# Optimization experiments

Measured on AMD Instinct MI355X. Metric: run time of the kernel, lower is better.

Reference implementation:

```python
import jax, jax.numpy as jnp
import numpy as np

B, S, H, I, C = 1024, 512, 128, 1, 10


def _uniform(key, shape, fan):
    stdv = 1.0 / np.sqrt(fan)
    return jax.random.uniform(key, shape, jnp.float32, -stdv, stdv)


def setup_inputs() -> dict:
    key = jax.random.key(0)
    ks = jax.random.split(key, 16)
    return {
        "x": jax.random.normal(ks[0], (B, S), jnp.float32),
        "W_gx": _uniform(ks[1], (I, H), H),
        "W_gh": _uniform(ks[2], (H, H), H),
        "W_ix": _uniform(ks[3], (I, H), H),
        "W_ih": _uniform(ks[4], (H, H), H),
        "W_fx": _uniform(ks[5], (I, H), H),
        "W_fh": _uniform(ks[6], (H, H), H),
        "W_ox": _uniform(ks[7], (I, H), H),
        "W_oh": _uniform(ks[8], (H, H), H),
        "W_ph": _uniform(ks[9], (H, C), C),
        "b_g": _uniform(ks[10], (H,), 1),
        "b_i": _uniform(ks[11], (H,), 1),
        "b_f": _uniform(ks[12], (H,), 1),
        "b_o": _uniform(ks[13], (H,), 1),
        "b_p": _uniform(ks[14], (C,), 1),
    }


def reference(x, W_gx, W_gh, W_ix, W_ih, W_fx, W_fh, W_ox, W_oh, W_ph,
              b_g, b_i, b_f, b_o, b_p):
    Hd = W_gh.shape[0]
    # Fuse the four per-gate GEMMs into one (same math, concatenated weights).
    Wx = jnp.concatenate([W_gx, W_ix, W_fx, W_ox], axis=1)   # [I, 4H]
    Wh = jnp.concatenate([W_gh, W_ih, W_fh, W_oh], axis=1)   # [H, 4H]
    b = jnp.concatenate([b_g, b_i, b_f, b_o])                # [4H]
    # input_dim == 1: timestep t input is x[:, t:t+1] -> xs: [S, B, 1]
    xs = jnp.swapaxes(x[:, :, None], 0, 1)
    # Precompute all input projections in one big GEMM: [S, B, 4H]
    xp = xs @ Wx + b

    def step(carry, xp_t):
        h, c = carry
        gates = xp_t + h @ Wh                    # [B, 4H]
        g = jnp.tanh(gates[:, :Hd])
        i = jax.nn.sigmoid(gates[:, Hd:2 * Hd])
        f = jax.nn.sigmoid(gates[:, 2 * Hd:3 * Hd])
        o = jax.nn.sigmoid(gates[:, 3 * Hd:])
        c_t = g * i + c * f
        h_t = jnp.tanh(c_t) * o
        return (h_t, c_t), None

    h0 = jnp.zeros((x.shape[0], Hd), x.dtype)
    (h_last, _), _ = jax.lax.scan(step, (h0, h0), xp)
    return h_last @ W_ph + b_p                   # logits at final timestep
```

## Files before the change

kernel.cpp:

```cpp
#include <hip/hip_runtime.h>

#define S_LEN 512
#define H_DIM 128
#define C_DIM 10

typedef __attribute__((ext_vector_type(8))) short short8;
typedef __attribute__((ext_vector_type(4))) float f32x4;

__device__ __forceinline__ unsigned short f2bf(float f) {
    union { float f; unsigned u; } v; v.f = f;
    return (unsigned short)((v.u + 0x7FFFu + ((v.u >> 16) & 1u)) >> 16);
}

__device__ __forceinline__ float fast_sigmoid(float x) {
    float e = __builtin_amdgcn_exp2f(-1.4426950408889634f * x);
    return __builtin_amdgcn_rcpf(1.0f + e);
}
__device__ __forceinline__ float fast_tanh(float x) {
    float e = __builtin_amdgcn_exp2f(2.8853900817779268f * x);
    return 1.0f - 2.0f * __builtin_amdgcn_rcpf(e + 1.0f);
}

__global__ __launch_bounds__(512, 2) void lstm_fused(
    const float* __restrict__ x,
    const float* __restrict__ Wgx, const float* __restrict__ Wgh,
    const float* __restrict__ Wix, const float* __restrict__ Wih,
    const float* __restrict__ Wfx, const float* __restrict__ Wfh,
    const float* __restrict__ Wox, const float* __restrict__ Woh,
    const float* __restrict__ Wph,
    const float* __restrict__ bg, const float* __restrict__ bi,
    const float* __restrict__ bff, const float* __restrict__ bo,
    const float* __restrict__ bp,
    float* __restrict__ out)
{
    __shared__ float xT[S_LEN][5];
    __shared__ __attribute__((aligned(16))) unsigned short hb[2][4][136];
    __shared__ float hfin[4][H_DIM];

    const int tid  = threadIdx.x;
    const int lane = tid & 63;
    const int w    = tid >> 6;
    const int b0   = blockIdx.x * 4;

    {
        const float* xp = x + b0 * S_LEN + tid;
        #pragma unroll
        for (int r = 0; r < 4; ++r) xT[tid][r] = xp[r * S_LEN];
    }
    {
        unsigned short* hz = &hb[0][0][0];
        for (int i2 = tid; i2 < 4 * 136; i2 += 512) hz[i2] = 0;
    }

    const int jl = lane & 15;
    const int kg = lane >> 4;
    const int j  = w * 16 + jl;

    const float* WhA[4] = { Wgh, Wih, Wfh, Woh };
    short8 bfrag[4][4];
    #pragma unroll
    for (int g = 0; g < 4; ++g) {
        #pragma unroll
        for (int kk = 0; kk < 4; ++kk) {
            const float* src = WhA[g] + (kk * 32 + kg * 8) * H_DIM + j;
            short8 v;
            #pragma unroll
            for (int e = 0; e < 8; ++e) v[e] = (short)f2bf(src[e * H_DIM]);
            bfrag[g][kk] = v;
        }
    }
    const float wxv[4] = { Wgx[j], Wix[j], Wfx[j], Wox[j] };
    const float bv[4]  = { bg[j],  bi[j],  bff[j], bo[j]  };

    const bool aActive = (lane & 3) == 0;
    const int  abase   = ((lane & 15) >> 2) * 272 + (lane >> 4) * 16;

    float cst  = 0.f;
    float hcur = 0.f;

    short8 afr[4];
    #pragma unroll
    for (int kk = 0; kk < 4; ++kk) afr[kk] = short8{0,0,0,0,0,0,0,0};

    __syncthreads();

    auto step = [&](int t, const unsigned short* src, unsigned short* dst) {
        if (aActive) {
            const char* base = (const char*)src + abase;
            #pragma unroll
            for (int kk = 0; kk < 4; ++kk)
                afr[kk] = *(const short8*)(base + kk * 64);
        }
        f32x4 acc[4] = {};
        #pragma unroll
        for (int kk = 0; kk < 4; ++kk) {
            #pragma unroll
            for (int g = 0; g < 4; ++g)
                acc[g] = __builtin_amdgcn_mfma_f32_16x16x32_bf16(
                             afr[kk], bfrag[g][kk], acc[g], 0, 0, 0);
        }
        const float xv = xT[t][kg];
        const float pg = acc[0][0] + xv * wxv[0] + bv[0];
        const float pi = acc[1][0] + xv * wxv[1] + bv[1];
        const float pf = acc[2][0] + xv * wxv[2] + bv[2];
        const float po = acc[3][0] + xv * wxv[3] + bv[3];
        const float cn = fast_tanh(pg) * fast_sigmoid(pi) + cst * fast_sigmoid(pf);
        cst = cn;
        hcur = fast_tanh(cn) * fast_sigmoid(po);
        *((unsigned short*)dst + kg * 136 + j) = f2bf(hcur);
        __syncthreads();
    };

    for (int t = 0; t < S_LEN; t += 2) {
        step(t,     &hb[0][0][0], &hb[1][0][0]);
        step(t + 1, &hb[1][0][0], &hb[0][0][0]);
    }

    hfin[kg][j] = hcur;
    __syncthreads();

    if (tid < 4 * C_DIM) {
        const int b = tid / C_DIM, cc = tid % C_DIM;
        float s = bp[cc];
        #pragma unroll 4
        for (int k = 0; k < H_DIM; ++k) s += hfin[b][k] * Wph[k * C_DIM + cc];
        out[(b0 + b) * C_DIM + cc] = s;
    }
}

extern "C" void kernel_launch(void* const* d_in, const int* in_sizes, int n_in,
                              void* d_out, int out_size, void* d_ws, size_t ws_size,
                              hipStream_t stream) {
    const float* x   = (const float*)d_in[0];
    const float* Wgx = (const float*)d_in[1];
    const float* Wgh = (const float*)d_in[2];
    const float* Wix = (const float*)d_in[3];
    const float* Wih = (const float*)d_in[4];
    const float* Wfx = (const float*)d_in[5];
    const float* Wfh = (const float*)d_in[6];
    const float* Wox = (const float*)d_in[7];
    const float* Woh = (const float*)d_in[8];
    const float* Wph = (const float*)d_in[9];
    const float* bg  = (const float*)d_in[10];
    const float* bi  = (const float*)d_in[11];
    const float* bf  = (const float*)d_in[12];
    const float* bo  = (const float*)d_in[13];
    const float* bp  = (const float*)d_in[14];
    float* out = (float*)d_out;

    lstm_fused<<<dim3(256), dim3(512), 0, stream>>>(
        x, Wgx, Wgh, Wix, Wih, Wfx, Wfh, Wox, Woh, Wph,
        bg, bi, bf, bo, bp, out);
}
```

Before: 218.0 us.

## Repack hidden-state LDS layout, split MFMA chains, and vectorize x loads

Stores the bf16 hidden state in a layout that matches the MFMA A-fragment order, so each active lane reads contiguous 16-byte chunks. Writes are packed two values per 32-bit store using a lane shuffle and v_cvt_pk_bf16_f32. The MFMA accumulation is split into two independent chains per gate to shorten the dependency chain. The x inputs are stored row-major and read four timesteps at a time with a single vector load. The aim is to cut the per-step serial latency of LDS traffic and MFMA dependencies in the recurrent loop, at the cost of an extra shuffle and an inline-asm dependency.

```diff
diff --git a/kernel.cpp b/kernel.cpp
--- a/kernel.cpp
+++ b/kernel.cpp
@@ -33,8 +33,8 @@
     const float* __restrict__ bp,
     float* __restrict__ out)
 {
-    __shared__ float xT[S_LEN][5];
-    __shared__ __attribute__((aligned(16))) unsigned short hb[2][4][136];
+    __shared__ float xr[4][516];
+    __shared__ __attribute__((aligned(16))) unsigned short hb[2][512];
     __shared__ float hfin[4][H_DIM];
 
     const int tid  = threadIdx.x;
@@ -45,12 +45,9 @@
     {
         const float* xp = x + b0 * S_LEN + tid;
         #pragma unroll
-        for (int r = 0; r < 4; ++r) xT[tid][r] = xp[r * S_LEN];
+        for (int r = 0; r < 4; ++r) xr[r][tid] = xp[r * S_LEN];
     }
-    {
-        unsigned short* hz = &hb[0][0][0];
-        for (int i2 = tid; i2 < 4 * 136; i2 += 512) hz[i2] = 0;
-    }
+    ((unsigned short*)hb)[tid] = 0;
 
     const int jl = lane & 15;
     const int kg = lane >> 4;
@@ -73,7 +70,10 @@
     const float bv[4]  = { bg[j],  bi[j],  bff[j], bo[j]  };
 
     const bool aActive = (lane & 3) == 0;
-    const int  abase   = ((lane & 15) >> 2) * 272 + (lane >> 4) * 16;
+    const int  abase   = (lane >> 2) * 16;
+
+    const bool wActive = (jl & 1) == 0;
+    const int  wbyte   = (j >> 5) * 256 + ((j >> 3) & 3) * 64 + kg * 16 + (j & 7) * 2;
 
     float cst  = 0.f;
     float hcur = 0.f;
@@ -84,36 +84,45 @@
 
     __syncthreads();
 
-    auto step = [&](int t, const unsigned short* src, unsigned short* dst) {
+    auto step = [&](const unsigned short* src, unsigned short* dst, float xv) {
         if (aActive) {
             const char* base = (const char*)src + abase;
             #pragma unroll
             for (int kk = 0; kk < 4; ++kk)
-                afr[kk] = *(const short8*)(base + kk * 64);
+                afr[kk] = *(const short8*)(base + kk * 256);
         }
-        f32x4 acc[4] = {};
+        f32x4 a0[4] = {}, a1[4] = {};
         #pragma unroll
-        for (int kk = 0; kk < 4; ++kk) {
-            #pragma unroll
-            for (int g = 0; g < 4; ++g)
-                acc[g] = __builtin_amdgcn_mfma_f32_16x16x32_bf16(
-                             afr[kk], bfrag[g][kk], acc[g], 0, 0, 0);
+        for (int g = 0; g < 4; ++g) {
+            a0[g] = __builtin_amdgcn_mfma_f32_16x16x32_bf16(afr[0], bfrag[g][0], a0[g], 0, 0, 0);
+            a1[g] = __builtin_amdgcn_mfma_f32_16x16x32_bf16(afr[2], bfrag[g][2], a1[g], 0, 0, 0);
+            a0[g] = __builtin_amdgcn_mfma_f32_16x16x32_bf16(afr[1], bfrag[g][1], a0[g], 0, 0, 0);
+            a1[g] = __builtin_amdgcn_mfma_f32_16x16x32_bf16(afr[3], bfrag[g][3], a1[g], 0, 0, 0);
         }
-        const float xv = xT[t][kg];
-        const float pg = acc[0][0] + xv * wxv[0] + bv[0];
-        const float pi = acc[1][0] + xv * wxv[1] + bv[1];
-        const float pf = acc[2][0] + xv * wxv[2] + bv[2];
-        const float po = acc[3][0] + xv * wxv[3] + bv[3];
+        const float pg = a0[0][0] + a1[0][0] + xv * wxv[0] + bv[0];
+        const float pi = a0[1][0] + a1[1][0] + xv * wxv[1] + bv[1];
+        const float pf = a0[2][0] + a1[2][0] + xv * wxv[2] + bv[2];
+        const float po = a0[3][0] + a1[3][0] + xv * wxv[3] + bv[3];
         const float cn = fast_tanh(pg) * fast_sigmoid(pi) + cst * fast_sigmoid(pf);
-        cst = cn;
+        cst  = cn;
         hcur = fast_tanh(cn) * fast_sigmoid(po);
-        *((unsigned short*)dst + kg * 136 + j) = f2bf(hcur);
+        const float hnb = __shfl_xor(hcur, 1);
+        if (wActive) {
+            unsigned pk;
+            asm("v_cvt_pk_bf16_f32 %0, %1, %2" : "=v"(pk) : "v"(hcur), "v"(hnb));
+            *(unsigned*)((char*)dst + wbyte) = pk;
+        }
         __syncthreads();
     };
 
-    for (int t = 0; t < S_LEN; t += 2) {
-        step(t,     &hb[0][0][0], &hb[1][0][0]);
-        step(t + 1, &hb[1][0][0], &hb[0][0][0]);
+    unsigned short* h0 = &hb[0][0];
+    unsigned short* h1 = &hb[1][0];
+    for (int t = 0; t < S_LEN; t += 4) {
+        const f32x4 xq = *(const f32x4*)&xr[kg][t];
+        step(h0, h1, xq[0]);
+        step(h1, h0, xq[1]);
+        step(h0, h1, xq[2]);
+        step(h1, h0, xq[3]);
     }
 
     hfin[kg][j] = hcur;
```

After: 237.6 us, median of 2. 1.09x slower.

## Halve block to 4 waves, each computing 32 hidden columns per step

Applied to the files above, without the earlier changes.

Each wave now owns two 16-column tiles of the hidden dimension, so the block shrinks from 8 to 4 waves. This halves the number of waves meeting at the per-timestep barrier and doubles the MFMA work per wave between barriers. The input projection and bias are folded into the MFMA accumulator init. x is loaded four timesteps at a time as a vector, h is packed to bf16 with a single conversion instruction, and the projection weights are staged in LDS. In exchange it uses more registers per wave (twice the B fragments) and less parallelism per block, which may lengthen each serial step.

```diff
diff --git a/kernel.cpp b/kernel.cpp
--- a/kernel.cpp
+++ b/kernel.cpp
@@ -21,7 +21,7 @@
     return 1.0f - 2.0f * __builtin_amdgcn_rcpf(e + 1.0f);
 }
 
-__global__ __launch_bounds__(512, 2) void lstm_fused(
+__global__ __launch_bounds__(256, 1) void lstm_fused(
     const float* __restrict__ x,
     const float* __restrict__ Wgx, const float* __restrict__ Wgh,
     const float* __restrict__ Wix, const float* __restrict__ Wih,
@@ -33,9 +33,10 @@
     const float* __restrict__ bp,
     float* __restrict__ out)
 {
-    __shared__ float xT[S_LEN][5];
-    __shared__ __attribute__((aligned(16))) unsigned short hb[2][4][136];
+    __shared__ float xr[4][516];
+    __shared__ __attribute__((aligned(16))) unsigned short hb[2][512];
     __shared__ float hfin[4][H_DIM];
+    __shared__ float wls[H_DIM * C_DIM];
 
     const int tid  = threadIdx.x;
     const int lane = tid & 63;
@@ -43,87 +44,128 @@
     const int b0   = blockIdx.x * 4;
 
     {
-        const float* xp = x + b0 * S_LEN + tid;
+        const float* xp = x + b0 * S_LEN;
         #pragma unroll
-        for (int r = 0; r < 4; ++r) xT[tid][r] = xp[r * S_LEN];
+        for (int r = 0; r < 4; ++r) {
+            xr[r][tid]       = xp[r * S_LEN + tid];
+            xr[r][tid + 256] = xp[r * S_LEN + tid + 256];
+        }
     }
-    {
-        unsigned short* hz = &hb[0][0][0];
-        for (int i2 = tid; i2 < 4 * 136; i2 += 512) hz[i2] = 0;
-    }
+    ((unsigned*)hb)[tid] = 0;
 
     const int jl = lane & 15;
     const int kg = lane >> 4;
-    const int j  = w * 16 + jl;
+    const int c0 = w * 32 + jl;
 
     const float* WhA[4] = { Wgh, Wih, Wfh, Woh };
-    short8 bfrag[4][4];
+    short8 bfrag[2][4][4];
     #pragma unroll
-    for (int g = 0; g < 4; ++g) {
+    for (int n = 0; n < 2; ++n) {
         #pragma unroll
-        for (int kk = 0; kk < 4; ++kk) {
-            const float* src = WhA[g] + (kk * 32 + kg * 8) * H_DIM + j;
-            short8 v;
+        for (int g = 0; g < 4; ++g) {
             #pragma unroll
-            for (int e = 0; e < 8; ++e) v[e] = (short)f2bf(src[e * H_DIM]);
-            bfrag[g][kk] = v;
+            for (int kk = 0; kk < 4; ++kk) {
+                const float* src = WhA[g] + (kk * 32 + kg * 8) * H_DIM + (w * 32 + 16 * n + jl);
+                short8 v;
+                #pragma unroll
+                for (int e = 0; e < 8; ++e) v[e] = (short)f2bf(src[e * H_DIM]);
+                bfrag[n][g][kk] = v;
+            }
         }
     }
-    const float wxv[4] = { Wgx[j], Wix[j], Wfx[j], Wox[j] };
-    const float bv[4]  = { bg[j],  bi[j],  bff[j], bo[j]  };
+    float wxv[2][4], bv[2][4];
+    {
+        const float* WxA[4] = { Wgx, Wix, Wfx, Wox };
+        const float* bA[4]  = { bg,  bi,  bff, bo  };
+        #pragma unroll
+        for (int n = 0; n < 2; ++n) {
+            #pragma unroll
+            for (int g = 0; g < 4; ++g) {
+                wxv[n][g] = WxA[g][c0 + 16 * n];
+                bv[n][g]  = bA[g][c0 + 16 * n];
+            }
+        }
+    }
 
     const bool aActive = (lane & 3) == 0;
-    const int  abase   = ((lane & 15) >> 2) * 272 + (lane >> 4) * 16;
+    const int  abase   = (lane >> 2) * 16;
+    const int  wbyte0  = (4 * w + (jl >> 3)) * 64 + kg * 16 + (jl & 7) * 2;
 
-    float cst  = 0.f;
-    float hcur = 0.f;
+    float cst[2] = { 0.f, 0.f };
+    float hcv[2] = { 0.f, 0.f };
 
     short8 afr[4];
     #pragma unroll
     for (int kk = 0; kk < 4; ++kk) afr[kk] = short8{0,0,0,0,0,0,0,0};
 
+    f32x4 acc[2][4];
+    #pragma unroll
+    for (int n = 0; n < 2; ++n)
+        #pragma unroll
+        for (int g = 0; g < 4; ++g) acc[n][g] = f32x4{0.f,0.f,0.f,0.f};
+
     __syncthreads();
 
-    auto step = [&](int t, const unsigned short* src, unsigned short* dst) {
-        if (aActive) {
-            const char* base = (const char*)src + abase;
+    unsigned short* const hp[2] = { &hb[0][0], &hb[1][0] };
+
+    for (int t4 = 0; t4 < S_LEN; t4 += 4) {
+        const f32x4 xq = *(const f32x4*)&xr[kg][t4];
+        #pragma unroll
+        for (int s = 0; s < 4; ++s) {
+            const unsigned short* src = hp[s & 1];
+            unsigned short*       dst = hp[(s & 1) ^ 1];
+            const float xv = xq[s];
+
+            #pragma unroll
+            for (int n = 0; n < 2; ++n)
+                #pragma unroll
+                for (int g = 0; g < 4; ++g)
+                    acc[n][g][0] = __builtin_fmaf(xv, wxv[n][g], bv[n][g]);
+
+            if (aActive) {
+                const char* base = (const char*)src + abase;
+                #pragma unroll
+                for (int kk = 0; kk < 4; ++kk)
+                    afr[kk] = *(const short8*)(base + kk * 256);
+            }
+
             #pragma unroll
             for (int kk = 0; kk < 4; ++kk)
-                afr[kk] = *(const short8*)(base + kk * 64);
+                #pragma unroll
+                for (int n = 0; n < 2; ++n)
+                    #pragma unroll
+                    for (int g = 0; g < 4; ++g)
+                        acc[n][g] = __builtin_amdgcn_mfma_f32_16x16x32_bf16(
+                                        afr[kk], bfrag[n][g][kk], acc[n][g], 0, 0, 0);
+
+            #pragma unroll
+            for (int n = 0; n < 2; ++n) {
+                const float tg = fast_tanh(acc[n][0][0]);
+                const float si = fast_sigmoid(acc[n][1][0]);
+                const float sf = fast_sigmoid(acc[n][2][0]);
+                const float so = fast_sigmoid(acc[n][3][0]);
+                const float cn = __builtin_fmaf(cst[n], sf, tg * si);
+                cst[n] = cn;
+                const float hn = fast_tanh(cn) * so;
+                hcv[n] = hn;
+                unsigned pk;
+                asm("v_cvt_pk_bf16_f32 %0, %1, %2" : "=v"(pk) : "v"(hn), "v"(hn));
+                *(unsigned short*)((char*)dst + wbyte0 + n * 128) = (unsigned short)pk;
+            }
+            __syncthreads();
         }
-        f32x4 acc[4] = {};
-        #pragma unroll
-        for (int kk = 0; kk < 4; ++kk) {
-            #pragma unroll
-            for (int g = 0; g < 4; ++g)
-                acc[g] = __builtin_amdgcn_mfma_f32_16x16x32_bf16(
-                             afr[kk], bfrag[g][kk], acc[g], 0, 0, 0);
-        }
-        const float xv = xT[t][kg];
-        const float pg = acc[0][0] + xv * wxv[0] + bv[0];
-        const float pi = acc[1][0] + xv * wxv[1] + bv[1];
-        const float pf = acc[2][0] + xv * wxv[2] + bv[2];
-        const float po = acc[3][0] + xv * wxv[3] + bv[3];
-        const float cn = fast_tanh(pg) * fast_sigmoid(pi) + cst * fast_sigmoid(pf);
-        cst = cn;
-        hcur = fast_tanh(cn) * fast_sigmoid(po);
-        *((unsigned short*)dst + kg * 136 + j) = f2bf(hcur);
-        __syncthreads();
-    };
-
-    for (int t = 0; t < S_LEN; t += 2) {
-        step(t,     &hb[0][0][0], &hb[1][0][0]);
-        step(t + 1, &hb[1][0][0], &hb[0][0][0]);
     }
 
-    hfin[kg][j] = hcur;
+    hfin[kg][c0]      = hcv[0];
+    hfin[kg][c0 + 16] = hcv[1];
+    for (int i = tid; i < H_DIM * C_DIM; i += 256) wls[i] = Wph[i];
     __syncthreads();
 
     if (tid < 4 * C_DIM) {
         const int b = tid / C_DIM, cc = tid % C_DIM;
         float s = bp[cc];
-        #pragma unroll 4
-        for (int k = 0; k < H_DIM; ++k) s += hfin[b][k] * Wph[k * C_DIM + cc];
+        #pragma unroll 8
+        for (int k = 0; k < H_DIM; ++k) s += hfin[b][k] * wls[k * C_DIM + cc];
         out[(b0 + b) * C_DIM + cc] = s;
     }
 }
@@ -148,7 +190,7 @@
     const float* bp  = (const float*)d_in[14];
     float* out = (float*)d_out;
 
-    lstm_fused<<<dim3(256), dim3(512), 0, stream>>>(
+    lstm_fused<<<dim3(256), dim3(256), 0, stream>>>(
         x, Wgx, Wgh, Wix, Wih, Wfx, Wfh, Wox, Woh, Wph,
         bg, bi, bf, bo, bp, out);
 }
```

Result: slower. 294.1 us (+34.9%).
